# Kernel tuning notes

Measured on AMD Instinct MI355X. Metric: run time of the kernel, lower is better.

Reference implementation:

```python
import jax, jax.numpy as jnp
import numpy as np

# dims: M=512 new tokens, N=2048 model dim, D=128 head dim, H=16 heads,
# L=4096 cache length, P=2048 cache write offset

def setup_inputs() -> dict:
    key = jax.random.key(0)
    k0, k1, k2, k3 = jax.random.split(key, 4)
    M, N, D, L = 512, 2048, 128, 4096
    X = jax.random.normal(k0, (M, N), jnp.float32)
    # scale weights ~1/sqrt(N) so projections have unit-ish scale
    W_qkv = jax.random.normal(k1, (N, 3 * N), jnp.float32) * (N ** -0.5)
    H = N // D
    cache_K = jax.random.normal(k2, (H, L, D), jnp.float32)
    # realistic cache state: keys stored in cache are RMS-normalized
    cache_K = cache_K * jax.lax.rsqrt(jnp.mean(cache_K * cache_K, axis=-1, keepdims=True))
    cache_V = jax.random.normal(k3, (H, L, D), jnp.float32)
    return {"X": X, "W_qkv": W_qkv, "cache_K": cache_K, "cache_V": cache_V, "P": 2048}


def reference(X, W_qkv, cache_K, cache_V, P):
    M = X.shape[0]
    H, L, D = cache_K.shape
    qkv = X @ W_qkv                              # [M, 3N]
    q, k, v = jnp.split(qkv, 3, axis=-1)         # each [M, N]
    q = q.reshape(M, H, D).transpose(1, 0, 2)    # [H, M, D]
    k = k.reshape(M, H, D).transpose(1, 0, 2)
    v = v.reshape(M, H, D).transpose(1, 0, 2)
    # RMS-style normalization (no learned gain, no eps in original)
    q = q * jax.lax.rsqrt(jnp.mean(q * q, axis=-1, keepdims=True))
    k = k * jax.lax.rsqrt(jnp.mean(k * k, axis=-1, keepdims=True))
    # scatter-update into KV cache at position P
    Kc = jax.lax.dynamic_update_slice(cache_K, k, (0, P, 0))  # [H, L, D]
    Vc = jax.lax.dynamic_update_slice(cache_V, v, (0, P, 0))
    # unmasked, unscaled attention over the full cache (faithful to original:
    # plain exp/sum, no max-subtraction, no 1/sqrt(D))
    scores = jnp.einsum('hmd,hld->hml', q, Kc)   # [H, M, L]
    w = jnp.exp(scores)
    w = w / jnp.sum(w, axis=-1, keepdims=True)
    out = jnp.einsum('hml,hld->hmd', w, Vc)      # [H, M, D]
    return out.transpose(1, 0, 2).reshape(M, H * D)
```

## Files before the change

kernel.cpp:

```cpp
#include <hip/hip_runtime.h>
#include <math.h>

typedef _Float16 half_t;
typedef _Float16 half8 __attribute__((ext_vector_type(8)));
typedef _Float16 half4_t __attribute__((ext_vector_type(4)));
typedef _Float16 half2_t __attribute__((ext_vector_type(2)));
typedef float floatx4 __attribute__((ext_vector_type(4)));

#define M_TOK 512
#define N_DIM 2048
#define D_HEAD 128
#define H_HEADS 16
#define L_CACHE 4096
#define THREE_N 6144
#define NCHUNK 8
#define LCHUNK 512

__global__ __launch_bounds__(256) void prep_kernel(const float* __restrict__ cK,
                                                   const float* __restrict__ cV,
                                                   const float* __restrict__ W,
                                                   const float* __restrict__ X,
                                                   const int* __restrict__ Pp,
                                                   half_t* __restrict__ K16,
                                                   half_t* __restrict__ V16T,
                                                   half_t* __restrict__ W16T,
                                                   half_t* __restrict__ X16) {
    __shared__ half_t tile[32 * 68];
    int b = blockIdx.x;
    int t = threadIdx.x;

    if (b < 8192) {
        int l0 = (b & 511) * 8;
        const int P = *Pp;
        if (l0 >= P && l0 + 8 <= P + M_TOK) return;
        size_t i = ((size_t)b * 256 + t) * 4;
        float4 v = *(const float4*)(cK + i);
        half4_t h = {(half_t)v.x, (half_t)v.y, (half_t)v.z, (half_t)v.w};
        *(half4_t*)(K16 + i) = h;
        return;
    }
    b -= 8192;
    if (b < 1024) {
        size_t i = ((size_t)b * 256 + t) * 4;
        float4 v = *(const float4*)(X + i);
        half4_t h = {(half_t)v.x, (half_t)v.y, (half_t)v.z, (half_t)v.w};
        *(half4_t*)(X16 + i) = h;
        return;
    }
    b -= 1024;
    if (b < 4096) {
        int h = b >> 8;
        int rem = b & 255;
        int lt = rem >> 2, dt = rem & 3;
        int l0 = lt * 64, d0 = dt * 32;
        const int P = *Pp;
        if (l0 >= P && l0 + 64 <= P + M_TOK) return;
#pragma unroll
        for (int p = 0; p < 2; ++p) {
            int li = p * 32 + (t >> 3), c4 = (t & 7) * 4;
            float4 v = *(const float4*)(cV + ((size_t)h * L_CACHE + l0 + li) * D_HEAD + d0 + c4);
            tile[(c4 + 0) * 68 + li] = (half_t)v.x;
            tile[(c4 + 1) * 68 + li] = (half_t)v.y;
            tile[(c4 + 2) * 68 + li] = (half_t)v.z;
            tile[(c4 + 3) * 68 + li] = (half_t)v.w;
        }
        __syncthreads();
        {
            int d = t >> 3, lg = (t & 7) * 8;
            *(half8*)(V16T + ((size_t)h * D_HEAD + d0 + d) * L_CACHE + l0 + lg) =
                *(half8*)&tile[d * 68 + lg];
        }
        return;
    }
    b -= 4096;
    {
        int n0 = (b % 192) * 32, k0 = (b / 192) * 64;
#pragma unroll
        for (int p = 0; p < 2; ++p) {
            int ki = p * 32 + (t >> 3), c4 = (t & 7) * 4;
            float4 v = *(const float4*)(W + (size_t)(k0 + ki) * THREE_N + n0 + c4);
            tile[(c4 + 0) * 68 + ki] = (half_t)v.x;
            tile[(c4 + 1) * 68 + ki] = (half_t)v.y;
            tile[(c4 + 2) * 68 + ki] = (half_t)v.z;
            tile[(c4 + 3) * 68 + ki] = (half_t)v.w;
        }
        __syncthreads();
        {
            int n = t >> 3, kg = (t & 7) * 8;
            *(half8*)(W16T + (size_t)(n0 + n) * N_DIM + k0 + kg) = *(half8*)&tile[n * 68 + kg];
        }
    }
}

__global__ __launch_bounds__(256) void gemm_fused_kernel(const half_t* __restrict__ X16,
                                                         const half_t* __restrict__ W16T,
                                                         const int* __restrict__ Pp,
                                                         half_t* __restrict__ Q16,
                                                         half_t* __restrict__ K16,
                                                         half_t* __restrict__ V16T) {
    __shared__ half_t As[64 * 72];
    __shared__ half_t Bs[128 * 72];
    __shared__ half_t Vt[128 * 72];
    __shared__ float ssbuf[4][32];
    const int t = threadIdx.x;
    const int wid = t >> 6, lane = t & 63;
    const int quad = lane >> 4, ln = lane & 15;
    const int bx = blockIdx.x, by = blockIdx.y;
    const int m0 = by * 64, n0 = bx * 128;
    const int wm = (wid >> 1) * 32, wn = (wid & 1) * 64;

    floatx4 acc[2][4] = {};

    const int ar = t >> 3, ag = (t & 7) * 8;
    const int br = t >> 3, bg = (t & 7) * 8;

    for (int k0 = 0; k0 < N_DIM; k0 += 64) {
        __syncthreads();
#pragma unroll
        for (int p = 0; p < 2; ++p) {
            int r = ar + p * 32;
            *(half8*)&As[r * 72 + ag] =
                *(const half8*)(X16 + (size_t)(m0 + r) * N_DIM + k0 + ag);
        }
#pragma unroll
        for (int p = 0; p < 4; ++p) {
            int r = br + p * 32;
            *(half8*)&Bs[r * 72 + bg] =
                *(const half8*)(W16T + (size_t)(n0 + r) * N_DIM + k0 + bg);
        }
        __syncthreads();
#pragma unroll
        for (int kt = 0; kt < 2; ++kt) {
            half8 a[2], b[4];
#pragma unroll
            for (int i = 0; i < 2; ++i)
                a[i] = *(half8*)&As[(wm + i * 16 + ln) * 72 + kt * 32 + quad * 8];
#pragma unroll
            for (int j = 0; j < 4; ++j)
                b[j] = *(half8*)&Bs[(wn + j * 16 + ln) * 72 + kt * 32 + quad * 8];
#pragma unroll
            for (int i = 0; i < 2; ++i)
#pragma unroll
                for (int j = 0; j < 4; ++j)
                    acc[i][j] = __builtin_amdgcn_mfma_f32_16x16x32_f16(a[i], b[j], acc[i][j], 0, 0, 0);
        }
    }

    const int seg = bx >> 4, h = bx & 15;
    const int P = *Pp;

    if (seg < 2) {
        float ss[2][4], scale[2][4];
#pragma unroll
        for (int i = 0; i < 2; ++i)
#pragma unroll
            for (int r = 0; r < 4; ++r) {
                float s = 0.f;
#pragma unroll
                for (int j = 0; j < 4; ++j) s += acc[i][j][r] * acc[i][j][r];
#pragma unroll
                for (int msk = 1; msk < 16; msk <<= 1) s += __shfl_xor(s, msk, 64);
                ss[i][r] = s;
            }
        if (ln == 0) {
#pragma unroll
            for (int i = 0; i < 2; ++i)
#pragma unroll
                for (int r = 0; r < 4; ++r)
                    ssbuf[wid][i * 16 + quad * 4 + r] = ss[i][r];
        }
        __syncthreads();
#pragma unroll
        for (int i = 0; i < 2; ++i)
#pragma unroll
            for (int r = 0; r < 4; ++r)
                scale[i][r] =
                    rsqrtf((ss[i][r] + ssbuf[wid ^ 1][i * 16 + quad * 4 + r]) * (1.0f / 128.0f));
#pragma unroll
        for (int i = 0; i < 2; ++i) {
            int mbase = m0 + wm + i * 16 + quad * 4;
#pragma unroll
            for (int j = 0; j < 4; ++j) {
                int col = wn + j * 16 + ln;
#pragma unroll
                for (int r = 0; r < 4; ++r) {
                    int m = mbase + r;
                    half_t val = (half_t)(acc[i][j][r] * scale[i][r]);
                    if (seg == 0)
                        Q16[((size_t)h * M_TOK + m) * D_HEAD + col] = val;
                    else
                        K16[((size_t)h * L_CACHE + P + m) * D_HEAD + col] = val;
                }
            }
        }
    } else {
#pragma unroll
        for (int i = 0; i < 2; ++i) {
            int mbase = wm + i * 16 + quad * 4;
#pragma unroll
            for (int j = 0; j < 4; ++j) {
                int d = wn + j * 16 + ln;
#pragma unroll
                for (int r = 0; r < 4; ++r)
                    Vt[d * 72 + mbase + r] = (half_t)acc[i][j][r];
            }
        }
        __syncthreads();
#pragma unroll
        for (int p = 0; p < 4; ++p) {
            int s = p * 256 + t;
            int d = s >> 3, sg = s & 7;
            *(half8*)(V16T + ((size_t)h * D_HEAD + d) * L_CACHE + P + m0 + sg * 8) =
                *(half8*)&Vt[d * 72 + sg * 8];
        }
    }
}

__global__ __launch_bounds__(256) void attn_partial_kernel(const half_t* __restrict__ Q16,
                                                           const half_t* __restrict__ K16,
                                                           const half_t* __restrict__ V16T,
                                                           half_t* __restrict__ Opart,
                                                           float* __restrict__ mstat,
                                                           float* __restrict__ lstat) {
    __shared__ half_t Ks[64 * 136];
    __shared__ half_t Vs[128 * 72];
    __shared__ half_t Ps[4 * 2 * 16 * 72];
    const int t = threadIdx.x, w = t >> 6, lane = t & 63;
    const int quad = lane >> 4, ln = lane & 15;

    const int bid = blockIdx.x;
    const int xcd = bid & 7, slot = bid >> 3;
    const int pair = (xcd << 4) | (slot >> 2);
    const int h = pair & 15, c = pair >> 4, mi = slot & 3;
    const int mb = mi * 128;

    const half_t* Qh = Q16 + (size_t)h * M_TOK * D_HEAD;
    const half_t* Kh = K16 + (size_t)h * L_CACHE * D_HEAD;
    const half_t* Vh = V16T + (size_t)h * D_HEAD * L_CACHE;

    half8 qf[2][4];
#pragma unroll
    for (int s = 0; s < 2; ++s) {
        int m0 = mb + w * 32 + s * 16;
#pragma unroll
        for (int dt = 0; dt < 4; ++dt)
            qf[s][dt] = *(const half8*)(Qh + (size_t)(m0 + ln) * D_HEAD + dt * 32 + quad * 8);
    }

    floatx4 oacc[2][8] = {};
    float mrow[2] = {-INFINITY, -INFINITY};
    float lrow[2] = {0.f, 0.f};

    half_t* Pw = Ps + w * (2 * 16 * 72);

    const int l0base = c * LCHUNK;
    const int kr = t >> 4, kc = (t & 15) * 8;
    const int vr = t >> 3, vc = (t & 7) * 8;

    half8 kreg[4], vreg[4];
#pragma unroll
    for (int p = 0; p < 4; ++p) {
        kreg[p] = *(const half8*)(Kh + (size_t)(l0base + p * 16 + kr) * D_HEAD + kc);
        vreg[p] = *(const half8*)(Vh + (size_t)(p * 32 + vr) * L_CACHE + l0base + vc);
    }

    for (int it = 0; it < LCHUNK / 64; ++it) {
        __syncthreads();
#pragma unroll
        for (int p = 0; p < 4; ++p)
            *(half8*)&Ks[(p * 16 + kr) * 136 + kc] = kreg[p];
#pragma unroll
        for (int p = 0; p < 4; ++p)
            *(half8*)&Vs[(p * 32 + vr) * 72 + vc] = vreg[p];
        if (it + 1 < LCHUNK / 64) {
            int l1 = l0base + (it + 1) * 64;
#pragma unroll
            for (int p = 0; p < 4; ++p) {
                kreg[p] = *(const half8*)(Kh + (size_t)(l1 + p * 16 + kr) * D_HEAD + kc);
                vreg[p] = *(const half8*)(Vh + (size_t)(p * 32 + vr) * L_CACHE + l1 + vc);
            }
        }
        __syncthreads();

        floatx4 sacc[2][4] = {};
#pragma unroll
        for (int dt = 0; dt < 4; ++dt) {
            half8 kf[4];
#pragma unroll
            for (int nt = 0; nt < 4; ++nt)
                kf[nt] = *(half8*)&Ks[(nt * 16 + ln) * 136 + dt * 32 + quad * 8];
#pragma unroll
            for (int s = 0; s < 2; ++s)
#pragma unroll
                for (int nt = 0; nt < 4; ++nt)
                    sacc[s][nt] = __builtin_amdgcn_mfma_f32_16x16x32_f16(kf[nt], qf[s][dt], sacc[s][nt], 0, 0, 0);
        }

#pragma unroll
        for (int s = 0; s < 2; ++s) {
            float mx = sacc[s][0][0];
#pragma unroll
            for (int nt = 0; nt < 4; ++nt)
#pragma unroll
                for (int r = 0; r < 4; ++r) mx = fmaxf(mx, sacc[s][nt][r]);
            mx = fmaxf(mx, __shfl_xor(mx, 16));
            mx = fmaxf(mx, __shfl_xor(mx, 32));
            if (__ballot(mx > mrow[s])) {
                float mnew = fmaxf(mrow[s], mx);
                float alpha = __expf(mrow[s] - mnew);
                mrow[s] = mnew;
                lrow[s] *= alpha;
                float ar[4];
#pragma unroll
                for (int r = 0; r < 4; ++r) ar[r] = __shfl(alpha, quad * 4 + r, 16);
#pragma unroll
                for (int nt8 = 0; nt8 < 8; ++nt8)
#pragma unroll
                    for (int r = 0; r < 4; ++r) oacc[s][nt8][r] *= ar[r];
            }
            float psum = 0.f;
#pragma unroll
            for (int nt = 0; nt < 4; ++nt) {
                half4_t h4;
#pragma unroll
                for (int r = 0; r < 4; ++r) {
                    float p = __expf(sacc[s][nt][r] - mrow[s]);
                    psum += p;
                    h4[r] = (half_t)p;
                }
                *(half4_t*)&Pw[s * 1152 + ln * 72 + nt * 16 + quad * 4] = h4;
            }
            psum += __shfl_xor(psum, 16);
            psum += __shfl_xor(psum, 32);
            lrow[s] += psum;
        }

#pragma unroll
        for (int kt = 0; kt < 2; ++kt) {
            half8 a0 = *(half8*)&Pw[ln * 72 + kt * 32 + quad * 8];
            half8 a1 = *(half8*)&Pw[1152 + ln * 72 + kt * 32 + quad * 8];
#pragma unroll
            for (int nt8 = 0; nt8 < 8; ++nt8) {
                half8 b = *(half8*)&Vs[(nt8 * 16 + ln) * 72 + kt * 32 + quad * 8];
                oacc[0][nt8] = __builtin_amdgcn_mfma_f32_16x16x32_f16(a0, b, oacc[0][nt8], 0, 0, 0);
                oacc[1][nt8] = __builtin_amdgcn_mfma_f32_16x16x32_f16(a1, b, oacc[1][nt8], 0, 0, 0);
            }
        }
    }

    half_t* Oc = Opart + ((size_t)(c * H_HEADS + h) * M_TOK) * D_HEAD;
    float* ms = mstat + (size_t)(c * H_HEADS + h) * M_TOK;
    float* ls = lstat + (size_t)(c * H_HEADS + h) * M_TOK;
#pragma unroll
    for (int s = 0; s < 2; ++s) {
        int m0 = mb + w * 32 + s * 16;
#pragma unroll
        for (int nt8 = 0; nt8 < 8; ++nt8) {
            int col = nt8 * 16 + ln;
#pragma unroll
            for (int r = 0; r < 4; ++r)
                Oc[(size_t)(m0 + quad * 4 + r) * D_HEAD + col] = (half_t)oacc[s][nt8][r];
        }
        if (lane < 16) {
            ms[m0 + lane] = mrow[s];
            ls[m0 + lane] = lrow[s];
        }
    }
}

__global__ __launch_bounds__(256) void combine_kernel(const half_t* __restrict__ Opart,
                                                      const float* __restrict__ mstat,
                                                      const float* __restrict__ lstat,
                                                      float* __restrict__ out) {
    int gw = blockIdx.x * 4 + (threadIdx.x >> 6);
    int lane = threadIdx.x & 63;
    int h = gw >> 9, m = gw & 511;
    int d = lane * 2;

    float ms[NCHUNK];
    float mg = -INFINITY;
#pragma unroll
    for (int c = 0; c < NCHUNK; ++c) {
        ms[c] = mstat[((c * H_HEADS + h) << 9) + m];
        mg = fmaxf(mg, ms[c]);
    }
    float denom = 0.f, o0 = 0.f, o1 = 0.f;
#pragma unroll
    for (int c = 0; c < NCHUNK; ++c) {
        float e = __expf(ms[c] - mg);
        denom += lstat[((c * H_HEADS + h) << 9) + m] * e;
        const half_t* Oc = Opart + (((size_t)(c * H_HEADS + h) << 9) + m) * D_HEAD + d;
        half2_t v = *(const half2_t*)Oc;
        o0 += (float)v.x * e;
        o1 += (float)v.y * e;
    }
    float inv = 1.0f / denom;
    float* op = out + (size_t)m * N_DIM + h * D_HEAD + d;
    op[0] = o0 * inv;
    op[1] = o1 * inv;
}

extern "C" void kernel_launch(void* const* d_in, const int* in_sizes, int n_in,
                              void* d_out, int out_size, void* d_ws, size_t ws_size,
                              hipStream_t stream) {
    const float* X = (const float*)d_in[0];
    const float* W = (const float*)d_in[1];
    const float* cK = (const float*)d_in[2];
    const float* cV = (const float*)d_in[3];
    const int* Pp = (const int*)d_in[4];
    float* out = (float*)d_out;

    char* ws = (char*)d_ws;
    half_t* Q16 = (half_t*)(ws + 0);
    half_t* K16 = (half_t*)(ws + 2097152);
    half_t* V16T = (half_t*)(ws + 18874368);
    half_t* X16 = (half_t*)(ws + 35651584);
    half_t* W16T = (half_t*)(ws + 37748736);
    half_t* Opart = (half_t*)(ws + 37748736);
    float* mstat = (float*)(ws + 71303168);
    float* lstat = (float*)(ws + 71827456);

    prep_kernel<<<19456, 256, 0, stream>>>(cK, cV, W, X, Pp, K16, V16T, W16T, X16);
    gemm_fused_kernel<<<dim3(48, 8), 256, 0, stream>>>(X16, W16T, Pp, Q16, K16, V16T);
    attn_partial_kernel<<<512, 256, 0, stream>>>(Q16, K16, V16T, Opart, mstat, lstat);
    combine_kernel<<<2048, 256, 0, stream>>>(Opart, mstat, lstat, out);
}
```

Baseline: 228.5 us.

## Halve attention row tile, XOR-swizzle LDS, and double per-block work in prep

The attention partial kernel now gives each wave 16 query rows instead of 32, so it launches twice as many blocks with smaller register and LDS footprints, and uses launch_bounds(256,4) to target higher occupancy. The unpadded LDS tiles for K, V and P now use XOR swizzles to avoid bank conflicts. The prep kernel handles twice as much data per block, with wider transpose tiles. The trade-off is that each K/V tile loaded into LDS is now reused by half as many query rows, which doubles K/V global traffic in the attention stage.

```diff
diff --git a/kernel.cpp b/kernel.cpp
--- a/kernel.cpp
+++ b/kernel.cpp
@@ -25,69 +25,88 @@
                                                    half_t* __restrict__ V16T,
                                                    half_t* __restrict__ W16T,
                                                    half_t* __restrict__ X16) {
-    __shared__ half_t tile[32 * 68];
+    __shared__ half_t tile[64 * 66];
     int b = blockIdx.x;
     int t = threadIdx.x;
 
-    if (b < 8192) {
-        int l0 = (b & 511) * 8;
+    if (b < 4096) {
+        int l0 = (b & 255) * 16;
         const int P = *Pp;
-        if (l0 >= P && l0 + 8 <= P + M_TOK) return;
-        size_t i = ((size_t)b * 256 + t) * 4;
-        float4 v = *(const float4*)(cK + i);
-        half4_t h = {(half_t)v.x, (half_t)v.y, (half_t)v.z, (half_t)v.w};
-        *(half4_t*)(K16 + i) = h;
+        if (l0 >= P && l0 + 16 <= P + M_TOK) return;
+        size_t i = (size_t)b * 2048 + t * 4;
+        float4 v0 = *(const float4*)(cK + i);
+        float4 v1 = *(const float4*)(cK + i + 1024);
+        half4_t h0 = {(half_t)v0.x, (half_t)v0.y, (half_t)v0.z, (half_t)v0.w};
+        half4_t h1 = {(half_t)v1.x, (half_t)v1.y, (half_t)v1.z, (half_t)v1.w};
+        *(half4_t*)(K16 + i) = h0;
+        *(half4_t*)(K16 + i + 1024) = h1;
         return;
     }
-    b -= 8192;
-    if (b < 1024) {
-        size_t i = ((size_t)b * 256 + t) * 4;
-        float4 v = *(const float4*)(X + i);
-        half4_t h = {(half_t)v.x, (half_t)v.y, (half_t)v.z, (half_t)v.w};
-        *(half4_t*)(X16 + i) = h;
+    b -= 4096;
+    if (b < 512) {
+        size_t i = (size_t)b * 2048 + t * 4;
+        float4 v0 = *(const float4*)(X + i);
+        float4 v1 = *(const float4*)(X + i + 1024);
+        half4_t h0 = {(half_t)v0.x, (half_t)v0.y, (half_t)v0.z, (half_t)v0.w};
+        half4_t h1 = {(half_t)v1.x, (half_t)v1.y, (half_t)v1.z, (half_t)v1.w};
+        *(half4_t*)(X16 + i) = h0;
+        *(half4_t*)(X16 + i + 1024) = h1;
         return;
     }
-    b -= 1024;
-    if (b < 4096) {
-        int h = b >> 8;
-        int rem = b & 255;
-        int lt = rem >> 2, dt = rem & 3;
-        int l0 = lt * 64, d0 = dt * 32;
+    b -= 512;
+    if (b < 2048) {
+        int h = b >> 7;
+        int rem = b & 127;
+        int lt = rem >> 1, dt = rem & 1;
+        int l0 = lt * 64, d0 = dt * 64;
         const int P = *Pp;
         if (l0 >= P && l0 + 64 <= P + M_TOK) return;
-#pragma unroll
-        for (int p = 0; p < 2; ++p) {
-            int li = p * 32 + (t >> 3), c4 = (t & 7) * 4;
-            float4 v = *(const float4*)(cV + ((size_t)h * L_CACHE + l0 + li) * D_HEAD + d0 + c4);
-            tile[(c4 + 0) * 68 + li] = (half_t)v.x;
-            tile[(c4 + 1) * 68 + li] = (half_t)v.y;
-            tile[(c4 + 2) * 68 + li] = (half_t)v.z;
-            tile[(c4 + 3) * 68 + li] = (half_t)v.w;
-        }
-        __syncthreads();
         {
-            int d = t >> 3, lg = (t & 7) * 8;
-            *(half8*)(V16T + ((size_t)h * D_HEAD + d0 + d) * L_CACHE + l0 + lg) =
-                *(half8*)&tile[d * 68 + lg];
+            int l = t >> 2, c0 = (t & 3) * 16;
+            const float* src = cV + ((size_t)h * L_CACHE + l0 + l) * D_HEAD + d0 + c0;
+            float4 v[4];
+#pragma unroll
+            for (int j = 0; j < 4; ++j) v[j] = *(const float4*)(src + j * 4);
+#pragma unroll
+            for (int j = 0; j < 4; ++j) {
+                tile[(c0 + j * 4 + 0) * 66 + l] = (half_t)v[j].x;
+                tile[(c0 + j * 4 + 1) * 66 + l] = (half_t)v[j].y;
+                tile[(c0 + j * 4 + 2) * 66 + l] = (half_t)v[j].z;
+                tile[(c0 + j * 4 + 3) * 66 + l] = (half_t)v[j].w;
+            }
+        }
+        __syncthreads();
+        {
+            int d = t >> 2, lg = (t & 3) * 16;
+            half_t* dst = V16T + ((size_t)h * D_HEAD + d0 + d) * L_CACHE + l0 + lg;
+            *(half8*)(dst) = *(half8*)&tile[d * 66 + lg];
+            *(half8*)(dst + 8) = *(half8*)&tile[d * 66 + lg + 8];
         }
         return;
     }
-    b -= 4096;
+    b -= 2048;
     {
-        int n0 = (b % 192) * 32, k0 = (b / 192) * 64;
-#pragma unroll
-        for (int p = 0; p < 2; ++p) {
-            int ki = p * 32 + (t >> 3), c4 = (t & 7) * 4;
-            float4 v = *(const float4*)(W + (size_t)(k0 + ki) * THREE_N + n0 + c4);
-            tile[(c4 + 0) * 68 + ki] = (half_t)v.x;
-            tile[(c4 + 1) * 68 + ki] = (half_t)v.y;
-            tile[(c4 + 2) * 68 + ki] = (half_t)v.z;
-            tile[(c4 + 3) * 68 + ki] = (half_t)v.w;
-        }
-        __syncthreads();
+        int n0 = (b % 96) * 64, k0 = (b / 96) * 64;
         {
-            int n = t >> 3, kg = (t & 7) * 8;
-            *(half8*)(W16T + (size_t)(n0 + n) * N_DIM + k0 + kg) = *(half8*)&tile[n * 68 + kg];
+            int k = t >> 2, c0 = (t & 3) * 16;
+            const float* src = W + (size_t)(k0 + k) * THREE_N + n0 + c0;
+            float4 v[4];
+#pragma unroll
+            for (int j = 0; j < 4; ++j) v[j] = *(const float4*)(src + j * 4);
+#pragma unroll
+            for (int j = 0; j < 4; ++j) {
+                tile[(c0 + j * 4 + 0) * 66 + k] = (half_t)v[j].x;
+                tile[(c0 + j * 4 + 1) * 66 + k] = (half_t)v[j].y;
+                tile[(c0 + j * 4 + 2) * 66 + k] = (half_t)v[j].z;
+                tile[(c0 + j * 4 + 3) * 66 + k] = (half_t)v[j].w;
+            }
+        }
+        __syncthreads();
+        {
+            int n = t >> 2, kg = (t & 3) * 16;
+            half_t* dst = W16T + (size_t)(n0 + n) * N_DIM + k0 + kg;
+            *(half8*)(dst) = *(half8*)&tile[n * 66 + kg];
+            *(half8*)(dst + 8) = *(half8*)&tile[n * 66 + kg + 8];
         }
     }
 }
@@ -216,46 +235,46 @@
     }
 }
 
-__global__ __launch_bounds__(256) void attn_partial_kernel(const half_t* __restrict__ Q16,
-                                                           const half_t* __restrict__ K16,
-                                                           const half_t* __restrict__ V16T,
-                                                           half_t* __restrict__ Opart,
-                                                           float* __restrict__ mstat,
-                                                           float* __restrict__ lstat) {
-    __shared__ half_t Ks[64 * 136];
-    __shared__ half_t Vs[128 * 72];
-    __shared__ half_t Ps[4 * 2 * 16 * 72];
+__global__ __launch_bounds__(256, 4) void attn_partial_kernel(const half_t* __restrict__ Q16,
+                                                              const half_t* __restrict__ K16,
+                                                              const half_t* __restrict__ V16T,
+                                                              half_t* __restrict__ Opart,
+                                                              float* __restrict__ mstat,
+                                                              float* __restrict__ lstat) {
+    __shared__ half_t Ks[64 * 128];
+    __shared__ half_t Vs[128 * 64];
+    __shared__ half_t Ps[4 * 16 * 64];
     const int t = threadIdx.x, w = t >> 6, lane = t & 63;
     const int quad = lane >> 4, ln = lane & 15;
 
     const int bid = blockIdx.x;
     const int xcd = bid & 7, slot = bid >> 3;
-    const int pair = (xcd << 4) | (slot >> 2);
-    const int h = pair & 15, c = pair >> 4, mi = slot & 3;
-    const int mb = mi * 128;
+    const int pair = (xcd << 4) | (slot >> 3);
+    const int h = pair & 15, c = pair >> 4, mi = slot & 7;
+    const int mb = mi * 64;
 
     const half_t* Qh = Q16 + (size_t)h * M_TOK * D_HEAD;
     const half_t* Kh = K16 + (size_t)h * L_CACHE * D_HEAD;
     const half_t* Vh = V16T + (size_t)h * D_HEAD * L_CACHE;
 
-    half8 qf[2][4];
-#pragma unroll
-    for (int s = 0; s < 2; ++s) {
-        int m0 = mb + w * 32 + s * 16;
-#pragma unroll
-        for (int dt = 0; dt < 4; ++dt)
-            qf[s][dt] = *(const half8*)(Qh + (size_t)(m0 + ln) * D_HEAD + dt * 32 + quad * 8);
-    }
-
-    floatx4 oacc[2][8] = {};
-    float mrow[2] = {-INFINITY, -INFINITY};
-    float lrow[2] = {0.f, 0.f};
-
-    half_t* Pw = Ps + w * (2 * 16 * 72);
+    const int m0 = mb + w * 16;
+    half8 qf[4];
+#pragma unroll
+    for (int dt = 0; dt < 4; ++dt)
+        qf[dt] = *(const half8*)(Qh + (size_t)(m0 + ln) * D_HEAD + dt * 32 + quad * 8);
+
+    floatx4 oacc[8] = {};
+    float mrow = -INFINITY;
+    float lrow = 0.f;
+
+    half_t* Pw = Ps + w * (16 * 64);
+    const int psw = (ln & 7) << 3;
 
     const int l0base = c * LCHUNK;
     const int kr = t >> 4, kc = (t & 15) * 8;
     const int vr = t >> 3, vc = (t & 7) * 8;
+    const int ksw = (kr & 7) << 3;
+    const int vsw = (vr & 7) << 3;
 
     half8 kreg[4], vreg[4];
 #pragma unroll
@@ -268,10 +287,10 @@
         __syncthreads();
 #pragma unroll
         for (int p = 0; p < 4; ++p)
-            *(half8*)&Ks[(p * 16 + kr) * 136 + kc] = kreg[p];
+            *(half8*)&Ks[(p * 16 + kr) * 128 + (kc ^ ksw)] = kreg[p];
 #pragma unroll
         for (int p = 0; p < 4; ++p)
-            *(half8*)&Vs[(p * 32 + vr) * 72 + vc] = vreg[p];
+            *(half8*)&Vs[(p * 32 + vr) * 64 + (vc ^ vsw)] = vreg[p];
         if (it + 1 < LCHUNK / 64) {
             int l1 = l0base + (it + 1) * 64;
 #pragma unroll
@@ -282,41 +301,38 @@
         }
         __syncthreads();
 
-        floatx4 sacc[2][4] = {};
+        floatx4 sacc[4] = {};
 #pragma unroll
         for (int dt = 0; dt < 4; ++dt) {
             half8 kf[4];
 #pragma unroll
             for (int nt = 0; nt < 4; ++nt)
-                kf[nt] = *(half8*)&Ks[(nt * 16 + ln) * 136 + dt * 32 + quad * 8];
-#pragma unroll
-            for (int s = 0; s < 2; ++s)
-#pragma unroll
-                for (int nt = 0; nt < 4; ++nt)
-                    sacc[s][nt] = __builtin_amdgcn_mfma_f32_16x16x32_f16(kf[nt], qf[s][dt], sacc[s][nt], 0, 0, 0);
-        }
-
-#pragma unroll
-        for (int s = 0; s < 2; ++s) {
-            float mx = sacc[s][0][0];
+                kf[nt] = *(half8*)&Ks[(nt * 16 + ln) * 128 + ((dt * 32 + quad * 8) ^ psw)];
 #pragma unroll
             for (int nt = 0; nt < 4; ++nt)
-#pragma unroll
-                for (int r = 0; r < 4; ++r) mx = fmaxf(mx, sacc[s][nt][r]);
+                sacc[nt] = __builtin_amdgcn_mfma_f32_16x16x32_f16(kf[nt], qf[dt], sacc[nt], 0, 0, 0);
+        }
+
+        {
+            float mx = sacc[0][0];
+#pragma unroll
+            for (int nt = 0; nt < 4; ++nt)
+#pragma unroll
+                for (int r = 0; r < 4; ++r) mx = fmaxf(mx, sacc[nt][r]);
             mx = fmaxf(mx, __shfl_xor(mx, 16));
             mx = fmaxf(mx, __shfl_xor(mx, 32));
-            if (__ballot(mx > mrow[s])) {
-                float mnew = fmaxf(mrow[s], mx);
-                float alpha = __expf(mrow[s] - mnew);
-                mrow[s] = mnew;
-                lrow[s] *= alpha;
+            if (__ballot(mx > mrow)) {
+                float mnew = fmaxf(mrow, mx);
+                float alpha = __expf(mrow - mnew);
+                mrow = mnew;
+                lrow *= alpha;
                 float ar[4];
 #pragma unroll
                 for (int r = 0; r < 4; ++r) ar[r] = __shfl(alpha, quad * 4 + r, 16);
 #pragma unroll
                 for (int nt8 = 0; nt8 < 8; ++nt8)
 #pragma unroll
-                    for (int r = 0; r < 4; ++r) oacc[s][nt8][r] *= ar[r];
+                    for (int r = 0; r < 4; ++r) oacc[nt8][r] *= ar[r];
             }
             float psum = 0.f;
 #pragma unroll
@@ -324,26 +340,24 @@
                 half4_t h4;
 #pragma unroll
                 for (int r = 0; r < 4; ++r) {
-                    float p = __expf(sacc[s][nt][r] - mrow[s]);
+                    float p = __expf(sacc[nt][r] - mrow);
                     psum += p;
                     h4[r] = (half_t)p;
                 }
-                *(half4_t*)&Pw[s * 1152 + ln * 72 + nt * 16 + quad * 4] = h4;
+                *(half4_t*)&Pw[ln * 64 + ((nt * 16 + quad * 4) ^ psw)] = h4;
             }
             psum += __shfl_xor(psum, 16);
             psum += __shfl_xor(psum, 32);
-            lrow[s] += psum;
+            lrow += psum;
         }
 
 #pragma unroll
         for (int kt = 0; kt < 2; ++kt) {
-            half8 a0 = *(half8*)&Pw[ln * 72 + kt * 32 + quad * 8];
-            half8 a1 = *(half8*)&Pw[1152 + ln * 72 + kt * 32 + quad * 8];
+            half8 a = *(half8*)&Pw[ln * 64 + ((kt * 32 + quad * 8) ^ psw)];
 #pragma unroll
             for (int nt8 = 0; nt8 < 8; ++nt8) {
-                half8 b = *(half8*)&Vs[(nt8 * 16 + ln) * 72 + kt * 32 + quad * 8];
-                oacc[0][nt8] = __builtin_amdgcn_mfma_f32_16x16x32_f16(a0, b, oacc[0][nt8], 0, 0, 0);
-                oacc[1][nt8] = __builtin_amdgcn_mfma_f32_16x16x32_f16(a1, b, oacc[1][nt8], 0, 0, 0);
+                half8 b = *(half8*)&Vs[(nt8 * 16 + ln) * 64 + ((kt * 32 + quad * 8) ^ psw)];
+                oacc[nt8] = __builtin_amdgcn_mfma_f32_16x16x32_f16(a, b, oacc[nt8], 0, 0, 0);
             }
         }
     }
@@ -352,19 +366,15 @@
     float* ms = mstat + (size_t)(c * H_HEADS + h) * M_TOK;
     float* ls = lstat + (size_t)(c * H_HEADS + h) * M_TOK;
 #pragma unroll
-    for (int s = 0; s < 2; ++s) {
-        int m0 = mb + w * 32 + s * 16;
-#pragma unroll
-        for (int nt8 = 0; nt8 < 8; ++nt8) {
-            int col = nt8 * 16 + ln;
-#pragma unroll
-            for (int r = 0; r < 4; ++r)
-                Oc[(size_t)(m0 + quad * 4 + r) * D_HEAD + col] = (half_t)oacc[s][nt8][r];
-        }
-        if (lane < 16) {
-            ms[m0 + lane] = mrow[s];
-            ls[m0 + lane] = lrow[s];
-        }
+    for (int nt8 = 0; nt8 < 8; ++nt8) {
+        int col = nt8 * 16 + ln;
+#pragma unroll
+        for (int r = 0; r < 4; ++r)
+            Oc[(size_t)(m0 + quad * 4 + r) * D_HEAD + col] = (half_t)oacc[nt8][r];
+    }
+    if (lane < 16) {
+        ms[m0 + lane] = mrow;
+        ls[m0 + lane] = lrow;
     }
 }
 
@@ -420,8 +430,8 @@
     float* mstat = (float*)(ws + 71303168);
     float* lstat = (float*)(ws + 71827456);
 
-    prep_kernel<<<19456, 256, 0, stream>>>(cK, cV, W, X, Pp, K16, V16T, W16T, X16);
+    prep_kernel<<<9728, 256, 0, stream>>>(cK, cV, W, X, Pp, K16, V16T, W16T, X16);
     gemm_fused_kernel<<<dim3(48, 8), 256, 0, stream>>>(X16, W16T, Pp, Q16, K16, V16T);
-    attn_partial_kernel<<<512, 256, 0, stream>>>(Q16, K16, V16T, Opart, mstat, lstat);
+    attn_partial_kernel<<<1024, 256, 0, stream>>>(Q16, K16, V16T, Opart, mstat, lstat);
     combine_kernel<<<2048, 256, 0, stream>>>(Opart, mstat, lstat, out);
 }
```

Result: faster. 222.1 us (-2.8%).
